# Performance work log

Measured on AMD Instinct MI355X. Metric: run time of the kernel, lower is better.

## Reference

```python
import jax, jax.numpy as jnp
import numpy as np

N_NODES = 20000
N_EDGES = 320000
DIM_IN = 768
DIM_H = 512
S_HOPS = 3
NUM_GNNS = 4
NEG_SLOPE = 0.2  # DGL GATConv default


def setup_inputs() -> dict:
    key = jax.random.key(0)
    ks = jax.random.split(key, 12)
    feat = jax.random.normal(ks[0], (N_NODES, DIM_IN), dtype=jnp.float32)
    src = jax.random.randint(ks[1], (N_EDGES,), 0, N_NODES)
    dst = jax.random.randint(ks[2], (N_EDGES,), 0, N_NODES)
    # learned params
    fc_W = jax.random.normal(ks[3], (DIM_IN, DIM_H), dtype=jnp.float32) * 0.02
    fc_b = jnp.zeros((DIM_H,), dtype=jnp.float32)
    gat_W = jax.random.normal(ks[4], (NUM_GNNS, DIM_H, DIM_H), dtype=jnp.float32) * 0.02
    gat_al = jax.random.normal(ks[5], (NUM_GNNS, DIM_H), dtype=jnp.float32) * 0.1
    gat_ar = jax.random.normal(ks[6], (NUM_GNNS, DIM_H), dtype=jnp.float32) * 0.1
    gat_b = jnp.zeros((NUM_GNNS, DIM_H), dtype=jnp.float32)
    beta = jnp.ones((S_HOPS + 1,), dtype=jnp.float32)
    return {"feat": feat, "fc_W": fc_W, "fc_b": fc_b, "gat_W": gat_W,
            "gat_al": gat_al, "gat_ar": gat_ar, "gat_b": gat_b,
            "beta": beta, "src": src, "dst": dst}


def _gat_layer(h, W, a_l, a_r, b, src, dst):
    z = h @ W                                   # [N, DH]
    el = z @ a_l                                # [N]
    er = z @ a_r                                # [N]
    e = jax.nn.leaky_relu(el[src] + er[dst], NEG_SLOPE)  # [E]
    # edge softmax over incoming edges of each dst node
    m = jax.ops.segment_max(e, dst, num_segments=N_NODES)
    ex = jnp.exp(e - m[dst])
    denom = jax.ops.segment_sum(ex, dst, num_segments=N_NODES)
    alpha = ex / denom[dst]                     # [E]
    out = jax.ops.segment_sum(alpha[:, None] * z[src], dst, num_segments=N_NODES)
    return out + b


def reference(feat, fc_W, fc_b, gat_W, gat_al, gat_ar, gat_b, beta, src, dst):
    h = feat @ fc_W + fc_b                      # dim_in -> 512
    for l in range(NUM_GNNS):
        h = _gat_layer(h, gat_W[l], gat_al[l], gat_ar[l], gat_b[l], src, dst)
    # A_hat = A + I propagation; A_hat @ Z = scatter(Z[src] -> dst) + Z
    Z_prev = h
    Z = beta[0] * Z_prev                        # accumulated Z is computed but the
    for s in range(1, S_HOPS + 1):              # original module returns Z_prev
        Z_s = jax.ops.segment_sum(Z_prev[src], dst, num_segments=N_NODES) + Z_prev
        Z = Z + beta[s] * Z_s
        Z_prev = Z_s
    return Z_prev
```

## Files before the change

kernel.cpp:

```cpp
#include <hip/hip_runtime.h>
#include <math.h>

#define N_NODES 20000
#define M_PAD   20096
#define N_EDGES 320000
#define DIM_IN 768
#define DIM_H 512
#define NUM_GNNS 4
#define NEG_SLOPE 0.2f

#define GEMM_TILES 628
#define GEMM_GRID  632

#define SLC_GRID 5000

typedef __attribute__((ext_vector_type(8))) short short8;
typedef __attribute__((ext_vector_type(4))) float f32x4;
typedef __attribute__((ext_vector_type(4))) unsigned int u32x4;

#define GPTR(p) (const __attribute__((address_space(1))) void*)(p)
#define LPTR(p) (__attribute__((address_space(3))) void*)(p)

__device__ __forceinline__ float bf2f(unsigned int lo16) {
  return __uint_as_float(lo16 << 16);
}
__device__ __forceinline__ unsigned short f2bf(float f) {
  unsigned int u = __float_as_uint(f);
  u += 0x7FFFu + ((u >> 16) & 1u);
  return (unsigned short)(u >> 16);
}
__device__ __forceinline__ void unpack8(uint4 v, float* f) {
  f[0] = bf2f(v.x & 0xffffu); f[1] = bf2f(v.x >> 16);
  f[2] = bf2f(v.y & 0xffffu); f[3] = bf2f(v.y >> 16);
  f[4] = bf2f(v.z & 0xffffu); f[5] = bf2f(v.z >> 16);
  f[6] = bf2f(v.w & 0xffffu); f[7] = bf2f(v.w >> 16);
}
__device__ __forceinline__ uint4 pack8(const float* o) {
  uint4 pv;
  pv.x = (unsigned)f2bf(o[0]) | ((unsigned)f2bf(o[1]) << 16);
  pv.y = (unsigned)f2bf(o[2]) | ((unsigned)f2bf(o[3]) << 16);
  pv.z = (unsigned)f2bf(o[4]) | ((unsigned)f2bf(o[5]) << 16);
  pv.w = (unsigned)f2bf(o[6]) | ((unsigned)f2bf(o[7]) << 16);
  return pv;
}

__device__ __forceinline__ float waveReduceSum(float v) {
#pragma unroll
  for (int off = 32; off > 0; off >>= 1) v += __shfl_xor(v, off, 64);
  return v;
}
__device__ __forceinline__ float waveReduceMax(float v) {
#pragma unroll
  for (int off = 32; off > 0; off >>= 1) v = fmaxf(v, __shfl_xor(v, off, 64));
  return v;
}

__global__ __launch_bounds__(256) void gemm_mfma_bf16(
    const unsigned short* __restrict__ A,
    const unsigned short* __restrict__ Bt,
    const float* __restrict__ bias,
    unsigned short* __restrict__ Cbf,
    int K) {
  int bid = blockIdx.x;
  int tile = (bid & 7) * (GEMM_GRID / 8) + (bid >> 3);
  if (tile >= GEMM_TILES) return;
  int brow = tile >> 2;
  int bcol = tile & 3;

  __shared__ __align__(16) unsigned short As[128 * 32];
  __shared__ __align__(16) unsigned short Bs[128 * 32];
  int tid = threadIdx.x;
  int wave = tid >> 6, lane = tid & 63;
  int wm = wave >> 1, wn = wave & 1;

  int rl = lane >> 2;
  int kc = (lane & 3) ^ ((lane >> 3) & 3);
  int r0 = 32 * wave;
  const unsigned short* gA0 = A + (size_t)(brow * 128 + r0 + rl) * K + kc * 8;
  const unsigned short* gA1 = gA0 + (size_t)16 * K;
  const unsigned short* gB0 = Bt + (size_t)(bcol * 128 + r0 + rl) * K + kc * 8;
  const unsigned short* gB1 = gB0 + (size_t)16 * K;
  unsigned short* lA0 = As + r0 * 32;
  unsigned short* lA1 = As + (r0 + 16) * 32;
  unsigned short* lB0 = Bs + r0 * 32;
  unsigned short* lB1 = Bs + (r0 + 16) * 32;

  int mrow = lane & 15;
  int q = lane >> 4;
  int swz = (q ^ ((mrow >> 1) & 3)) * 8;
  const short8* ra = (const short8*)(As + (64 * wm + mrow) * 32 + swz);
  const short8* rb = (const short8*)(Bs + (64 * wn + mrow) * 32 + swz);

  f32x4 acc[4][4];
#pragma unroll
  for (int i = 0; i < 4; ++i)
#pragma unroll
    for (int j = 0; j < 4; ++j) acc[i][j] = (f32x4)(0.f);

  for (int k0 = 0; k0 < K; k0 += 32) {
    __syncthreads();
    __builtin_amdgcn_global_load_lds(GPTR(gA0 + k0), LPTR(lA0), 16, 0, 0);
    __builtin_amdgcn_global_load_lds(GPTR(gA1 + k0), LPTR(lA1), 16, 0, 0);
    __builtin_amdgcn_global_load_lds(GPTR(gB0 + k0), LPTR(lB0), 16, 0, 0);
    __builtin_amdgcn_global_load_lds(GPTR(gB1 + k0), LPTR(lB1), 16, 0, 0);
    __syncthreads();
    short8 a[4], b[4];
#pragma unroll
    for (int t = 0; t < 4; ++t) a[t] = ra[t * 64];
#pragma unroll
    for (int t = 0; t < 4; ++t) b[t] = rb[t * 64];
#pragma unroll
    for (int mt = 0; mt < 4; ++mt)
#pragma unroll
      for (int nt = 0; nt < 4; ++nt)
        acc[mt][nt] = __builtin_amdgcn_mfma_f32_16x16x32_bf16(a[mt], b[nt], acc[mt][nt], 0, 0, 0);
  }

  int colb = bcol * 128 + 64 * wn + (lane & 15);
  int rowb = brow * 128 + 64 * wm + 4 * q;
#pragma unroll
  for (int nt = 0; nt < 4; ++nt) {
    int col = colb + 16 * nt;
    float bv = bias ? bias[col] : 0.f;
#pragma unroll
    for (int mt = 0; mt < 4; ++mt) {
      int row = rowb + 16 * mt;
#pragma unroll
      for (int i = 0; i < 4; ++i)
        Cbf[(size_t)(row + i) * DIM_H + col] = f2bf(acc[mt][nt][i] + bv);
    }
  }
}

__global__ void convert_feat(const float* __restrict__ feat, unsigned short* __restrict__ Abf) {
  int t = blockIdx.x * blockDim.x + threadIdx.x;
  const int CHUNKS = M_PAD * DIM_IN / 8;
  if (t >= CHUNKS) return;
  int row = t / (DIM_IN / 8);
  uint4 o;
  if (row < N_NODES) {
    const float4* p = (const float4*)(feat + (size_t)t * 8);
    float4 x = p[0], y = p[1];
    o.x = (unsigned)f2bf(x.x) | ((unsigned)f2bf(x.y) << 16);
    o.y = (unsigned)f2bf(x.z) | ((unsigned)f2bf(x.w) << 16);
    o.z = (unsigned)f2bf(y.x) | ((unsigned)f2bf(y.y) << 16);
    o.w = (unsigned)f2bf(y.z) | ((unsigned)f2bf(y.w) << 16);
  } else {
    o = make_uint4(0, 0, 0, 0);
  }
  ((uint4*)Abf)[t] = o;
}

__global__ __launch_bounds__(256) void transpose_bf16(const float* __restrict__ in,
                                                      unsigned short* __restrict__ out,
                                                      int R, int C) {
  __shared__ float tile[32][33];
  int tx = threadIdx.x, ty = threadIdx.y;
  size_t base = (size_t)blockIdx.z * R * C;
  int r0 = blockIdx.x * 32, c0 = blockIdx.y * 32;
#pragma unroll
  for (int i = 0; i < 4; ++i) {
    int r = r0 + ty + i * 8;
    tile[ty + i * 8][tx] = in[base + (size_t)r * C + c0 + tx];
  }
  __syncthreads();
#pragma unroll
  for (int i = 0; i < 4; ++i) {
    int c = c0 + ty + i * 8;
    out[base + (size_t)c * R + r0 + tx] = f2bf(tile[tx][ty + i * 8]);
  }
}

__global__ void count_edges(const int* __restrict__ dst, int* __restrict__ counts) {
  int k = blockIdx.x * blockDim.x + threadIdx.x;
  if (k < N_EDGES) atomicAdd(&counts[dst[k]], 1);
}

__global__ __launch_bounds__(1024) void scan_kernel(const int* __restrict__ counts,
                                                    int* __restrict__ indptr) {
  __shared__ int part[1024];
  int tid = threadIdx.x;
  const int CH = (N_NODES + 1023) / 1024;
  int base = tid * CH;
  int s = 0;
  for (int i = 0; i < CH; ++i) {
    int idx = base + i;
    if (idx < N_NODES) s += counts[idx];
  }
  part[tid] = s;
  __syncthreads();
  for (int off = 1; off < 1024; off <<= 1) {
    int v = (tid >= off) ? part[tid - off] : 0;
    __syncthreads();
    part[tid] += v;
    __syncthreads();
  }
  int run = (tid == 0) ? 0 : part[tid - 1];
  for (int i = 0; i < CH; ++i) {
    int idx = base + i;
    if (idx < N_NODES) {
      indptr[idx] = run;
      run += counts[idx];
      if (idx == N_NODES - 1) indptr[N_NODES] = run;
    }
  }
}

__global__ void fill_adj(const int* __restrict__ src, const int* __restrict__ dst,
                         const int* __restrict__ indptr, int* __restrict__ cursor,
                         int* __restrict__ adjsrc) {
  int k = blockIdx.x * blockDim.x + threadIdx.x;
  if (k < N_EDGES) {
    int d = dst[k];
    int pos = atomicAdd(&cursor[d], 1);
    adjsrc[indptr[d] + pos] = src[k];
  }
}

__global__ __launch_bounds__(256) void eler_bf(const unsigned short* __restrict__ zbf,
                                               const float* __restrict__ al,
                                               const float* __restrict__ ar,
                                               float* __restrict__ el, float* __restrict__ er) {
  int wid = (blockIdx.x * blockDim.x + threadIdx.x) >> 6;
  int lane = threadIdx.x & 63;
  if (wid >= N_NODES) return;
  uint4 zv = ((const uint4*)(zbf + (size_t)wid * DIM_H))[lane];
  float z[8];
  unpack8(zv, z);
  const float4* al4 = (const float4*)(al + lane * 8);
  const float4* ar4 = (const float4*)(ar + lane * 8);
  float4 a0 = al4[0], a1 = al4[1], r0 = ar4[0], r1 = ar4[1];
  float sl = z[0] * a0.x + z[1] * a0.y + z[2] * a0.z + z[3] * a0.w +
             z[4] * a1.x + z[5] * a1.y + z[6] * a1.z + z[7] * a1.w;
  float sr = z[0] * r0.x + z[1] * r0.y + z[2] * r0.z + z[3] * r0.w +
             z[4] * r1.x + z[5] * r1.y + z[6] * r1.z + z[7] * r1.w;
  sl = waveReduceSum(sl);
  sr = waveReduceSum(sr);
  if (lane == 0) { el[wid] = sl; er[wid] = sr; }
}

__global__ __launch_bounds__(256) void edge_softmax_alpha(
    const float* __restrict__ el, const float* __restrict__ er,
    const int* __restrict__ indptr, const int* __restrict__ adjsrc,
    float* __restrict__ alpha) {
  int v = (blockIdx.x * blockDim.x + threadIdx.x) >> 6;
  int lane = threadIdx.x & 63;
  if (v >= N_NODES) return;
  int begin = indptr[v], end = indptr[v + 1];
  float er_v = er[v];

  float m = -INFINITY;
  for (int j = begin + lane; j < end; j += 64) {
    float e = el[adjsrc[j]] + er_v;
    e = (e >= 0.f) ? e : NEG_SLOPE * e;
    alpha[j] = e;
    m = fmaxf(m, e);
  }
  m = waveReduceMax(m);

  float ss = 0.f;
  for (int j = begin + lane; j < end; j += 64) {
    float ex = __expf(alpha[j] - m);
    alpha[j] = ex;
    ss += ex;
  }
  float denom = waveReduceSum(ss);
  float inv = (end > begin) ? 1.f / denom : 0.f;

  for (int j = begin + lane; j < end; j += 64) alpha[j] *= inv;
}

__global__ __launch_bounds__(256, 8) void gather_slc(
    const unsigned short* __restrict__ zin, const float* __restrict__ alpha,
    const int* __restrict__ indptr, const int* __restrict__ adjsrc,
    const float* __restrict__ bias, int self_term,
    unsigned short* __restrict__ out_bf, float* __restrict__ out_f32) {
  int slice = blockIdx.x & 7;
  int grp = blockIdx.x >> 3;
  int wave = threadIdx.x >> 6, lane = threadIdx.x & 63;
  int slot = lane >> 3, sub = lane & 7;
  int v = grp * 32 + wave * 8 + slot;
  unsigned cbyte = (unsigned)(slice * 128 + sub * 16);
  const char* zb = (const char*)zin;
  const char* ab = (const char*)adjsrc;
  const char* wb = (const char*)alpha;

  int b = indptr[v];
  unsigned ue = (unsigned)indptr[v + 1];
  int deg = (int)ue - b;
  int md = deg;
  md = max(md, __shfl_xor(md, 8, 64));
  md = max(md, __shfl_xor(md, 16, 64));
  md = max(md, __shfl_xor(md, 32, 64));

  float acc[8];
  if (self_term) {
    uint4 sz = *(const uint4*)(zb + (((unsigned)v) << 10) + cbyte);
    unpack8(sz, acc);
  } else {
#pragma unroll
    for (int i = 0; i < 8; ++i) acc[i] = 0.f;
  }

  unsigned jb = (unsigned)b;
  const unsigned EMAX = (unsigned)(N_EDGES - 1);
#pragma nounroll
  for (int t = 0; t < md; t += 4) {
    unsigned j0 = jb + (unsigned)t;
    unsigned a0 = min(j0 + 0u, EMAX) << 2;
    unsigned a1 = min(j0 + 1u, EMAX) << 2;
    unsigned a2 = min(j0 + 2u, EMAX) << 2;
    unsigned a3 = min(j0 + 3u, EMAX) << 2;
    int i0 = *(const int*)(ab + a0);
    int i1 = *(const int*)(ab + a1);
    int i2 = *(const int*)(ab + a2);
    int i3 = *(const int*)(ab + a3);
    float w0 = alpha ? *(const float*)(wb + a0) : 1.f;
    float w1 = alpha ? *(const float*)(wb + a1) : 1.f;
    float w2 = alpha ? *(const float*)(wb + a2) : 1.f;
    float w3 = alpha ? *(const float*)(wb + a3) : 1.f;
    w0 = (j0 + 0u < ue) ? w0 : 0.f;
    w1 = (j0 + 1u < ue) ? w1 : 0.f;
    w2 = (j0 + 2u < ue) ? w2 : 0.f;
    w3 = (j0 + 3u < ue) ? w3 : 0.f;
    uint4 z0 = *(const uint4*)(zb + (((unsigned)i0) << 10) + cbyte);
    uint4 z1 = *(const uint4*)(zb + (((unsigned)i1) << 10) + cbyte);
    uint4 z2 = *(const uint4*)(zb + (((unsigned)i2) << 10) + cbyte);
    uint4 z3 = *(const uint4*)(zb + (((unsigned)i3) << 10) + cbyte);
    float f0[8], f1[8], f2[8], f3[8];
    unpack8(z0, f0); unpack8(z1, f1); unpack8(z2, f2); unpack8(z3, f3);
#pragma unroll
    for (int i = 0; i < 8; ++i) {
      acc[i] = fmaf(w0, f0[i], acc[i]);
      acc[i] = fmaf(w1, f1[i], acc[i]);
      acc[i] = fmaf(w2, f2[i], acc[i]);
      acc[i] = fmaf(w3, f3[i], acc[i]);
    }
  }

  if (bias) {
    const float4* b4 = (const float4*)(bias + slice * 64 + sub * 8);
    float4 b0 = b4[0], b1 = b4[1];
    acc[0] += b0.x; acc[1] += b0.y; acc[2] += b0.z; acc[3] += b0.w;
    acc[4] += b1.x; acc[5] += b1.y; acc[6] += b1.z; acc[7] += b1.w;
  }
  if (out_bf) {
    uint4 pv = pack8(acc);
    *(uint4*)((char*)out_bf + (((unsigned)v) << 10) + cbyte) = pv;
  } else {
    char* p = (char*)out_f32 + (((unsigned)v) << 11) + cbyte * 2;
    *(f32x4*)p = (f32x4){acc[0], acc[1], acc[2], acc[3]};
    *(f32x4*)(p + 16) = (f32x4){acc[4], acc[5], acc[6], acc[7]};
  }
}

extern "C" void kernel_launch(void* const* d_in, const int* in_sizes, int n_in,
                              void* d_out, int out_size, void* d_ws, size_t ws_size,
                              hipStream_t stream) {
  const float* feat = (const float*)d_in[0];
  const float* fc_W = (const float*)d_in[1];
  const float* fc_b = (const float*)d_in[2];
  const float* gat_W = (const float*)d_in[3];
  const float* gat_al = (const float*)d_in[4];
  const float* gat_ar = (const float*)d_in[5];
  const float* gat_b = (const float*)d_in[6];
  const int* src = (const int*)d_in[8];
  const int* dst = (const int*)d_in[9];
  float* out = (float*)d_out;

  char* w = (char*)d_ws;
  auto alloc = [&](size_t bytes) {
    char* p = w;
    w += (bytes + 255) & ~(size_t)255;
    return p;
  };
  unsigned short* hbf   = (unsigned short*)alloc((size_t)M_PAD * DIM_H * 2);
  unsigned short* fcWt  = (unsigned short*)alloc((size_t)DIM_H * DIM_IN * 2);
  unsigned short* gatWt = (unsigned short*)alloc((size_t)NUM_GNNS * DIM_H * DIM_H * 2);
  float* el    = (float*)alloc((size_t)N_NODES * 4);
  float* er    = (float*)alloc((size_t)N_NODES * 4);
  int* counts  = (int*)alloc((size_t)2 * N_NODES * 4);
  int* cursor  = counts + N_NODES;
  int* indptr  = (int*)alloc((size_t)(N_NODES + 1) * 4);
  int* adjsrc  = (int*)alloc((size_t)N_EDGES * 4);
  char* uni = alloc((size_t)M_PAD * DIM_IN * 2);
  unsigned short* Abf = (unsigned short*)uni;
  float* alpha = (float*)uni;
  unsigned short* Z1  = (unsigned short*)uni;
  unsigned short* zbf = (unsigned short*)d_out;

  hipMemsetAsync(counts, 0, sizeof(int) * 2 * N_NODES, stream);
  count_edges<<<(N_EDGES + 255) / 256, 256, 0, stream>>>(dst, counts);
  scan_kernel<<<1, 1024, 0, stream>>>(counts, indptr);
  fill_adj<<<(N_EDGES + 255) / 256, 256, 0, stream>>>(src, dst, indptr, cursor, adjsrc);

  convert_feat<<<(M_PAD * DIM_IN / 8 + 255) / 256, 256, 0, stream>>>(feat, Abf);
  transpose_bf16<<<dim3(DIM_IN / 32, DIM_H / 32, 1), dim3(32, 8), 0, stream>>>(fc_W, fcWt, DIM_IN, DIM_H);
  transpose_bf16<<<dim3(DIM_H / 32, DIM_H / 32, NUM_GNNS), dim3(32, 8), 0, stream>>>(gat_W, gatWt, DIM_H, DIM_H);

  gemm_mfma_bf16<<<GEMM_GRID, 256, 0, stream>>>(Abf, fcWt, fc_b, hbf, DIM_IN);

  int nwaveblocks = (N_NODES * 64 + 255) / 256;
  for (int l = 0; l < NUM_GNNS; ++l) {
    gemm_mfma_bf16<<<GEMM_GRID, 256, 0, stream>>>(hbf, gatWt + (size_t)l * DIM_H * DIM_H,
                                                  nullptr, zbf, DIM_H);
    eler_bf<<<nwaveblocks, 256, 0, stream>>>(zbf, gat_al + (size_t)l * DIM_H,
                                             gat_ar + (size_t)l * DIM_H, el, er);
    edge_softmax_alpha<<<nwaveblocks, 256, 0, stream>>>(el, er, indptr, adjsrc, alpha);
    gather_slc<<<SLC_GRID, 256, 0, stream>>>(
        zbf, alpha, indptr, adjsrc, gat_b + (size_t)l * DIM_H, 0, hbf, nullptr);
  }

  gather_slc<<<SLC_GRID, 256, 0, stream>>>(hbf, nullptr, indptr, adjsrc, nullptr, 1, Z1, nullptr);
  gather_slc<<<SLC_GRID, 256, 0, stream>>>(Z1, nullptr, indptr, adjsrc, nullptr, 1, hbf, nullptr);
  gather_slc<<<SLC_GRID, 256, 0, stream>>>(hbf, nullptr, indptr, adjsrc, nullptr, 1, nullptr, out);
}
```

Measured before the change: 582.5 us.

## Double-buffer GEMM LDS, degree-sort nodes, pack edge pairs, widen gather unroll

The GEMM now double-buffers its LDS tiles so the next K-slice loads while MFMAs run. It also stages the output tile through LDS to make coalesced 16-byte stores. Nodes are bucket-sorted by in-degree into a permutation, so the 8 nodes sharing a wave have similar degrees and less loop divergence. The softmax writes packed (src, alpha) pairs, and the gather loop is unrolled to 8 edges with all loads issued up front. This raises register pressure (launch bounds hint removed) and adds a few small preprocessing kernels.

```diff
diff --git a/kernel.cpp b/kernel.cpp
--- a/kernel.cpp
+++ b/kernel.cpp
@@ -16,7 +16,6 @@
 
 typedef __attribute__((ext_vector_type(8))) short short8;
 typedef __attribute__((ext_vector_type(4))) float f32x4;
-typedef __attribute__((ext_vector_type(4))) unsigned int u32x4;
 
 #define GPTR(p) (const __attribute__((address_space(1))) void*)(p)
 #define LPTR(p) (__attribute__((address_space(3))) void*)(p)
@@ -67,8 +66,7 @@
   int brow = tile >> 2;
   int bcol = tile & 3;
 
-  __shared__ __align__(16) unsigned short As[128 * 32];
-  __shared__ __align__(16) unsigned short Bs[128 * 32];
+  __shared__ __align__(16) unsigned short lds[4][128 * 32];
   int tid = threadIdx.x;
   int wave = tid >> 6, lane = tid & 63;
   int wm = wave >> 1, wn = wave & 1;
@@ -80,16 +78,10 @@
   const unsigned short* gA1 = gA0 + (size_t)16 * K;
   const unsigned short* gB0 = Bt + (size_t)(bcol * 128 + r0 + rl) * K + kc * 8;
   const unsigned short* gB1 = gB0 + (size_t)16 * K;
-  unsigned short* lA0 = As + r0 * 32;
-  unsigned short* lA1 = As + (r0 + 16) * 32;
-  unsigned short* lB0 = Bs + r0 * 32;
-  unsigned short* lB1 = Bs + (r0 + 16) * 32;
 
   int mrow = lane & 15;
   int q = lane >> 4;
   int swz = (q ^ ((mrow >> 1) & 3)) * 8;
-  const short8* ra = (const short8*)(As + (64 * wm + mrow) * 32 + swz);
-  const short8* rb = (const short8*)(Bs + (64 * wn + mrow) * 32 + swz);
 
   f32x4 acc[4][4];
 #pragma unroll
@@ -97,38 +89,66 @@
 #pragma unroll
     for (int j = 0; j < 4; ++j) acc[i][j] = (f32x4)(0.f);
 
-  for (int k0 = 0; k0 < K; k0 += 32) {
-    __syncthreads();
-    __builtin_amdgcn_global_load_lds(GPTR(gA0 + k0), LPTR(lA0), 16, 0, 0);
-    __builtin_amdgcn_global_load_lds(GPTR(gA1 + k0), LPTR(lA1), 16, 0, 0);
-    __builtin_amdgcn_global_load_lds(GPTR(gB0 + k0), LPTR(lB0), 16, 0, 0);
-    __builtin_amdgcn_global_load_lds(GPTR(gB1 + k0), LPTR(lB1), 16, 0, 0);
-    __syncthreads();
+  int nk = K >> 5;
+  {
+    unsigned short* lA = lds[0] + r0 * 32;
+    unsigned short* lB = lds[2] + r0 * 32;
+    __builtin_amdgcn_global_load_lds(GPTR(gA0), LPTR(lA), 16, 0, 0);
+    __builtin_amdgcn_global_load_lds(GPTR(gA1), LPTR(lA + 512), 16, 0, 0);
+    __builtin_amdgcn_global_load_lds(GPTR(gB0), LPTR(lB), 16, 0, 0);
+    __builtin_amdgcn_global_load_lds(GPTR(gB1), LPTR(lB + 512), 16, 0, 0);
+  }
+  __syncthreads();
+
+  for (int t = 0; t < nk; ++t) {
+    int cur = t & 1;
+    if (t + 1 < nk) {
+      int k0 = (t + 1) << 5;
+      unsigned short* lA = lds[cur ^ 1] + r0 * 32;
+      unsigned short* lB = lds[2 + (cur ^ 1)] + r0 * 32;
+      __builtin_amdgcn_global_load_lds(GPTR(gA0 + k0), LPTR(lA), 16, 0, 0);
+      __builtin_amdgcn_global_load_lds(GPTR(gA1 + k0), LPTR(lA + 512), 16, 0, 0);
+      __builtin_amdgcn_global_load_lds(GPTR(gB0 + k0), LPTR(lB), 16, 0, 0);
+      __builtin_amdgcn_global_load_lds(GPTR(gB1 + k0), LPTR(lB + 512), 16, 0, 0);
+    }
+    const short8* ra = (const short8*)(lds[cur] + (64 * wm + mrow) * 32 + swz);
+    const short8* rb = (const short8*)(lds[2 + cur] + (64 * wn + mrow) * 32 + swz);
     short8 a[4], b[4];
 #pragma unroll
-    for (int t = 0; t < 4; ++t) a[t] = ra[t * 64];
-#pragma unroll
-    for (int t = 0; t < 4; ++t) b[t] = rb[t * 64];
+    for (int u = 0; u < 4; ++u) a[u] = ra[u * 64];
+#pragma unroll
+    for (int u = 0; u < 4; ++u) b[u] = rb[u * 64];
 #pragma unroll
     for (int mt = 0; mt < 4; ++mt)
 #pragma unroll
       for (int nt = 0; nt < 4; ++nt)
         acc[mt][nt] = __builtin_amdgcn_mfma_f32_16x16x32_bf16(a[mt], b[nt], acc[mt][nt], 0, 0, 0);
-  }
-
-  int colb = bcol * 128 + 64 * wn + (lane & 15);
-  int rowb = brow * 128 + 64 * wm + 4 * q;
-#pragma unroll
-  for (int nt = 0; nt < 4; ++nt) {
-    int col = colb + 16 * nt;
-    float bv = bias ? bias[col] : 0.f;
-#pragma unroll
-    for (int mt = 0; mt < 4; ++mt) {
-      int row = rowb + 16 * mt;
-#pragma unroll
-      for (int i = 0; i < 4; ++i)
-        Cbf[(size_t)(row + i) * DIM_H + col] = f2bf(acc[mt][nt][i] + bv);
-    }
+    __syncthreads();
+  }
+
+  unsigned short* Cs = lds[0];
+  {
+    float bv[4];
+#pragma unroll
+    for (int nt = 0; nt < 4; ++nt)
+      bv[nt] = bias ? bias[bcol * 128 + 64 * wn + 16 * nt + mrow] : 0.f;
+#pragma unroll
+    for (int mt = 0; mt < 4; ++mt)
+#pragma unroll
+      for (int nt = 0; nt < 4; ++nt)
+#pragma unroll
+        for (int i = 0; i < 4; ++i) {
+          int row = 64 * wm + 16 * mt + 4 * q + i;
+          int col = 64 * wn + 16 * nt + mrow;
+          Cs[row * 128 + col] = f2bf(acc[mt][nt][i] + bv[nt]);
+        }
+  }
+  __syncthreads();
+  int rr = tid >> 4, cb = (tid & 15) * 8;
+#pragma unroll
+  for (int it = 0; it < 8; ++it, rr += 16) {
+    uint4 val = *(const uint4*)(Cs + rr * 128 + cb);
+    *(uint4*)(Cbf + (size_t)(brow * 128 + rr) * DIM_H + bcol * 128 + cb) = val;
   }
 }
 
@@ -214,6 +234,26 @@
     int d = dst[k];
     int pos = atomicAdd(&cursor[d], 1);
     adjsrc[indptr[d] + pos] = src[k];
+  }
+}
+
+__global__ void hist64(const int* __restrict__ counts, int* __restrict__ hist) {
+  int v = blockIdx.x * blockDim.x + threadIdx.x;
+  if (v < N_NODES) atomicAdd(&hist[min(counts[v], 63)], 1);
+}
+__global__ void scan64(const int* __restrict__ hist, int* __restrict__ base) {
+  if (threadIdx.x == 0) {
+    int run = 0;
+    for (int i = 0; i < 64; ++i) { base[i] = run; run += hist[i]; }
+  }
+}
+__global__ void scatter_perm(const int* __restrict__ counts, int* __restrict__ base,
+                             int* __restrict__ perm) {
+  int v = blockIdx.x * blockDim.x + threadIdx.x;
+  if (v < N_NODES) {
+    int b = min(counts[v], 63);
+    int pos = atomicAdd(&base[b], 1);
+    perm[pos] = v;
   }
 }
 
@@ -242,7 +282,7 @@
 __global__ __launch_bounds__(256) void edge_softmax_alpha(
     const float* __restrict__ el, const float* __restrict__ er,
     const int* __restrict__ indptr, const int* __restrict__ adjsrc,
-    float* __restrict__ alpha) {
+    float* __restrict__ alpha, int2* __restrict__ apairs) {
   int v = (blockIdx.x * blockDim.x + threadIdx.x) >> 6;
   int lane = threadIdx.x & 63;
   if (v >= N_NODES) return;
@@ -267,28 +307,27 @@
   float denom = waveReduceSum(ss);
   float inv = (end > begin) ? 1.f / denom : 0.f;
 
-  for (int j = begin + lane; j < end; j += 64) alpha[j] *= inv;
-}
-
-__global__ __launch_bounds__(256, 8) void gather_slc(
-    const unsigned short* __restrict__ zin, const float* __restrict__ alpha,
+  for (int j = begin + lane; j < end; j += 64)
+    apairs[j] = make_int2(adjsrc[j], __float_as_int(alpha[j] * inv));
+}
+
+__global__ __launch_bounds__(256) void gather_slc(
+    const unsigned short* __restrict__ zin, const int2* __restrict__ apairs,
     const int* __restrict__ indptr, const int* __restrict__ adjsrc,
-    const float* __restrict__ bias, int self_term,
+    const int* __restrict__ perm, const float* __restrict__ bias, int self_term,
     unsigned short* __restrict__ out_bf, float* __restrict__ out_f32) {
   int slice = blockIdx.x & 7;
   int grp = blockIdx.x >> 3;
   int wave = threadIdx.x >> 6, lane = threadIdx.x & 63;
   int slot = lane >> 3, sub = lane & 7;
-  int v = grp * 32 + wave * 8 + slot;
+  int vidx = grp * 32 + wave * 8 + slot;
+  int v = perm[vidx];
   unsigned cbyte = (unsigned)(slice * 128 + sub * 16);
   const char* zb = (const char*)zin;
-  const char* ab = (const char*)adjsrc;
-  const char* wb = (const char*)alpha;
 
   int b = indptr[v];
   unsigned ue = (unsigned)indptr[v + 1];
-  int deg = (int)ue - b;
-  int md = deg;
+  int md = (int)ue - b;
   md = max(md, __shfl_xor(md, 8, 64));
   md = max(md, __shfl_xor(md, 16, 64));
   md = max(md, __shfl_xor(md, 32, 64));
@@ -304,37 +343,56 @@
 
   unsigned jb = (unsigned)b;
   const unsigned EMAX = (unsigned)(N_EDGES - 1);
+  if (apairs) {
+    const char* pb = (const char*)apairs;
 #pragma nounroll
-  for (int t = 0; t < md; t += 4) {
-    unsigned j0 = jb + (unsigned)t;
-    unsigned a0 = min(j0 + 0u, EMAX) << 2;
-    unsigned a1 = min(j0 + 1u, EMAX) << 2;
-    unsigned a2 = min(j0 + 2u, EMAX) << 2;
-    unsigned a3 = min(j0 + 3u, EMAX) << 2;
-    int i0 = *(const int*)(ab + a0);
-    int i1 = *(const int*)(ab + a1);
-    int i2 = *(const int*)(ab + a2);
-    int i3 = *(const int*)(ab + a3);
-    float w0 = alpha ? *(const float*)(wb + a0) : 1.f;
-    float w1 = alpha ? *(const float*)(wb + a1) : 1.f;
-    float w2 = alpha ? *(const float*)(wb + a2) : 1.f;
-    float w3 = alpha ? *(const float*)(wb + a3) : 1.f;
-    w0 = (j0 + 0u < ue) ? w0 : 0.f;
-    w1 = (j0 + 1u < ue) ? w1 : 0.f;
-    w2 = (j0 + 2u < ue) ? w2 : 0.f;
-    w3 = (j0 + 3u < ue) ? w3 : 0.f;
-    uint4 z0 = *(const uint4*)(zb + (((unsigned)i0) << 10) + cbyte);
-    uint4 z1 = *(const uint4*)(zb + (((unsigned)i1) << 10) + cbyte);
-    uint4 z2 = *(const uint4*)(zb + (((unsigned)i2) << 10) + cbyte);
-    uint4 z3 = *(const uint4*)(zb + (((unsigned)i3) << 10) + cbyte);
-    float f0[8], f1[8], f2[8], f3[8];
-    unpack8(z0, f0); unpack8(z1, f1); unpack8(z2, f2); unpack8(z3, f3);
-#pragma unroll
-    for (int i = 0; i < 8; ++i) {
-      acc[i] = fmaf(w0, f0[i], acc[i]);
-      acc[i] = fmaf(w1, f1[i], acc[i]);
-      acc[i] = fmaf(w2, f2[i], acc[i]);
-      acc[i] = fmaf(w3, f3[i], acc[i]);
+    for (int t = 0; t < md; t += 8) {
+      unsigned j0 = jb + (unsigned)t;
+      int idx[8];
+      float wv[8];
+#pragma unroll
+      for (int u = 0; u < 8; ++u) {
+        unsigned a = min(j0 + (unsigned)u, EMAX) << 3;
+        int2 p = *(const int2*)(pb + a);
+        idx[u] = p.x;
+        wv[u] = (j0 + (unsigned)u < ue) ? __int_as_float(p.y) : 0.f;
+      }
+      uint4 z[8];
+#pragma unroll
+      for (int u = 0; u < 8; ++u)
+        z[u] = *(const uint4*)(zb + (((unsigned)idx[u]) << 10) + cbyte);
+#pragma unroll
+      for (int u = 0; u < 8; ++u) {
+        float f[8];
+        unpack8(z[u], f);
+#pragma unroll
+        for (int i = 0; i < 8; ++i) acc[i] = fmaf(wv[u], f[i], acc[i]);
+      }
+    }
+  } else {
+    const char* ab = (const char*)adjsrc;
+#pragma nounroll
+    for (int t = 0; t < md; t += 8) {
+      unsigned j0 = jb + (unsigned)t;
+      int idx[8];
+      float wv[8];
+#pragma unroll
+      for (int u = 0; u < 8; ++u) {
+        unsigned a = min(j0 + (unsigned)u, EMAX) << 2;
+        idx[u] = *(const int*)(ab + a);
+        wv[u] = (j0 + (unsigned)u < ue) ? 1.f : 0.f;
+      }
+      uint4 z[8];
+#pragma unroll
+      for (int u = 0; u < 8; ++u)
+        z[u] = *(const uint4*)(zb + (((unsigned)idx[u]) << 10) + cbyte);
+#pragma unroll
+      for (int u = 0; u < 8; ++u) {
+        float f[8];
+        unpack8(z[u], f);
+#pragma unroll
+        for (int i = 0; i < 8; ++i) acc[i] = fmaf(wv[u], f[i], acc[i]);
+      }
     }
   }
 
@@ -379,20 +437,27 @@
   unsigned short* gatWt = (unsigned short*)alloc((size_t)NUM_GNNS * DIM_H * DIM_H * 2);
   float* el    = (float*)alloc((size_t)N_NODES * 4);
   float* er    = (float*)alloc((size_t)N_NODES * 4);
-  int* counts  = (int*)alloc((size_t)2 * N_NODES * 4);
+  int* counts  = (int*)alloc((size_t)(2 * N_NODES + 128) * 4);
   int* cursor  = counts + N_NODES;
+  int* hist    = counts + 2 * N_NODES;
+  int* basebuf = hist + 64;
   int* indptr  = (int*)alloc((size_t)(N_NODES + 1) * 4);
   int* adjsrc  = (int*)alloc((size_t)N_EDGES * 4);
+  int* perm    = (int*)alloc((size_t)N_NODES * 4);
   char* uni = alloc((size_t)M_PAD * DIM_IN * 2);
   unsigned short* Abf = (unsigned short*)uni;
   float* alpha = (float*)uni;
+  int2* apairs = (int2*)(uni + (((size_t)N_EDGES * 4 + 255) & ~(size_t)255));
   unsigned short* Z1  = (unsigned short*)uni;
   unsigned short* zbf = (unsigned short*)d_out;
 
-  hipMemsetAsync(counts, 0, sizeof(int) * 2 * N_NODES, stream);
+  hipMemsetAsync(counts, 0, sizeof(int) * (2 * N_NODES + 128), stream);
   count_edges<<<(N_EDGES + 255) / 256, 256, 0, stream>>>(dst, counts);
   scan_kernel<<<1, 1024, 0, stream>>>(counts, indptr);
   fill_adj<<<(N_EDGES + 255) / 256, 256, 0, stream>>>(src, dst, indptr, cursor, adjsrc);
+  hist64<<<(N_NODES + 255) / 256, 256, 0, stream>>>(counts, hist);
+  scan64<<<1, 64, 0, stream>>>(hist, basebuf);
+  scatter_perm<<<(N_NODES + 255) / 256, 256, 0, stream>>>(counts, basebuf, perm);
 
   convert_feat<<<(M_PAD * DIM_IN / 8 + 255) / 256, 256, 0, stream>>>(feat, Abf);
   transpose_bf16<<<dim3(DIM_IN / 32, DIM_H / 32, 1), dim3(32, 8), 0, stream>>>(fc_W, fcWt, DIM_IN, DIM_H);
@@ -406,12 +471,12 @@
                                                   nullptr, zbf, DIM_H);
     eler_bf<<<nwaveblocks, 256, 0, stream>>>(zbf, gat_al + (size_t)l * DIM_H,
                                              gat_ar + (size_t)l * DIM_H, el, er);
-    edge_softmax_alpha<<<nwaveblocks, 256, 0, stream>>>(el, er, indptr, adjsrc, alpha);
+    edge_softmax_alpha<<<nwaveblocks, 256, 0, stream>>>(el, er, indptr, adjsrc, alpha, apairs);
     gather_slc<<<SLC_GRID, 256, 0, stream>>>(
-        zbf, alpha, indptr, adjsrc, gat_b + (size_t)l * DIM_H, 0, hbf, nullptr);
-  }
-
-  gather_slc<<<SLC_GRID, 256, 0, stream>>>(hbf, nullptr, indptr, adjsrc, nullptr, 1, Z1, nullptr);
-  gather_slc<<<SLC_GRID, 256, 0, stream>>>(Z1, nullptr, indptr, adjsrc, nullptr, 1, hbf, nullptr);
-  gather_slc<<<SLC_GRID, 256, 0, stream>>>(hbf, nullptr, indptr, adjsrc, nullptr, 1, nullptr, out);
-}
+        zbf, apairs, indptr, adjsrc, perm, gat_b + (size_t)l * DIM_H, 0, hbf, nullptr);
+  }
+
+  gather_slc<<<SLC_GRID, 256, 0, stream>>>(hbf, nullptr, indptr, adjsrc, perm, nullptr, 1, Z1, nullptr);
+  gather_slc<<<SLC_GRID, 256, 0, stream>>>(Z1, nullptr, indptr, adjsrc, perm, nullptr, 1, hbf, nullptr);
+  gather_slc<<<SLC_GRID, 256, 0, stream>>>(hbf, nullptr, indptr, adjsrc, perm, nullptr, 1, nullptr, out);
+}
```

New measurement: 700.0 us. 20.2% more time.
